# Kernel tuning notes

Measured on AMD Instinct MI355X. Metric: run time of the kernel, lower is better.

Reference implementation:

```python
import jax, jax.numpy as jnp
import numpy as np

EPS = 1e-5

def conv3x3(x, w, b):
    # x: [B,C,H,W], w: [O,I,3,3], padding=1 (SAME)
    y = jax.lax.conv_general_dilated(x, w, window_strides=(1, 1),
                                     padding=[(1, 1), (1, 1)],
                                     dimension_numbers=('NCHW', 'OIHW', 'NCHW'))
    return y + b[None, :, None, None]

def pool_block(x, k):
    # exact adaptive avg pool: 300 is divisible by the output size, block size k
    B, C, H, W = x.shape
    return x.reshape(B, C, H // k, k, W // k, k).mean(axis=(3, 5))

def upsample_nearest(x, k):
    # equivalent to the nested python-loop slice-assign in RIA
    return jnp.repeat(jnp.repeat(x, k, axis=2), k, axis=3)

def _conv_param(key, o, i):
    k1, k2 = jax.random.split(key)
    fan_in = i * 9
    w = jax.random.normal(k1, (o, i, 3, 3), jnp.float32) * np.sqrt(2.0 / fan_in)
    b = jax.random.normal(k2, (o,), jnp.float32) * 0.01
    return w, b

def setup_inputs() -> dict:
    key = jax.random.key(0)
    ks = jax.random.split(key, 16)
    inp = {}
    inp['im'] = jax.random.normal(ks[0], (32, 3, 300, 300), jnp.float32)
    inp['w1'], inp['b1'] = _conv_param(ks[1], 8, 3)
    inp['w2'], inp['b2'] = _conv_param(ks[2], 16, 8)
    inp['w3'], inp['b3'] = _conv_param(ks[3], 32, 16)
    inp['w4'], inp['b4'] = _conv_param(ks[4], 16, 32)
    inp['w5'], inp['b5'] = _conv_param(ks[5], 8, 16)
    inp['wc5'], inp['bc5'] = _conv_param(ks[6], 8, 16)
    inp['wc10'], inp['bc10'] = _conv_param(ks[7], 8, 16)
    inp['wc15'], inp['bc15'] = _conv_param(ks[8], 8, 16)
    inp['wg'], inp['bg'] = _conv_param(ks[9], 8, 24)
    inp['wm'], inp['bm'] = _conv_param(ks[10], 8, 24)
    inp['bn_w'] = jnp.ones((8,), jnp.float32)
    inp['bn_b'] = jnp.zeros((8,), jnp.float32)
    inp['w11'], inp['b11'] = _conv_param(ks[11], 1, 8)
    inp['gamma'] = jnp.full((1,), 0.3, jnp.float32)
    return inp

def reference(im, w1, b1, w2, b2, w3, b3, w4, b4, w5, b5,
              wc5, bc5, wc10, bc10, wc15, bc15,
              wg, bg, wm, bm, bn_w, bn_b, w11, b11, gamma):
    # attention conv chain 3->8->16->32->16->8
    x = conv3x3(im, w1, b1)
    x = conv3x3(x, w2, b2)
    x = conv3x3(x, w3, b3)
    x = conv3x3(x, w4, b4)
    x = conv3x3(x, w5, b5)  # [B,8,300,300]

    # RIA: triple-scale pooled context, nearest-upsampled and fused
    up5 = upsample_nearest(pool_block(x, 5), 5)
    up10 = upsample_nearest(pool_block(x, 10), 10)
    up15 = upsample_nearest(pool_block(x, 15), 15)
    c5 = conv3x3(jnp.concatenate([x, up5], axis=1), wc5, bc5)
    c10 = conv3x3(jnp.concatenate([x, up10], axis=1), wc10, bc10)
    c15 = conv3x3(jnp.concatenate([x, up15], axis=1), wc15, bc15)
    g_in = jnp.concatenate([c5, c10, c15], axis=1)  # [B,24,300,300]

    # gated conv (activation=None): conv(x) * sigmoid(mask_conv(x)), then BN (batch stats)
    gated = conv3x3(g_in, wg, bg) * jax.nn.sigmoid(conv3x3(g_in, wm, bm))
    mean = gated.mean(axis=(0, 2, 3), keepdims=True)
    var = gated.var(axis=(0, 2, 3), keepdims=True)
    gated = (gated - mean) * jax.lax.rsqrt(var + EPS)
    gated = gated * bn_w[None, :, None, None] + bn_b[None, :, None, None]

    # 8->1 conv, sigmoid attention map, residual gating with gamma
    att = jax.nn.sigmoid(conv3x3(gated, w11, b11))  # [B,1,300,300]
    out = gamma * (att * im) + (1.0 - gamma) * im
    return out
```

## Files before the change

kernel.cpp:

```cpp
#include <hip/hip_runtime.h>
#include <hip/hip_bf16.h>
#include <math.h>

typedef __hip_bfloat16 bf16;
typedef __attribute__((ext_vector_type(8))) __bf16 bf16x8;
typedef __attribute__((ext_vector_type(8))) unsigned short u16x8;
typedef __attribute__((ext_vector_type(4))) float f32x4;

#define H_ 300
#define W_ 300
#define HW_ 90000
#define NBATCH 32
#define NPART (NBATCH * 190)
#define NPB 95

__device__ __forceinline__ float b2f(unsigned short u) {
    return __uint_as_float((unsigned int)u << 16);
}
__device__ __forceinline__ unsigned short f2u(float v) {
    bf16 b = __float2bfloat16(v);
    return *reinterpret_cast<unsigned short*>(&b);
}
__device__ __forceinline__ float sigm(float x) { return 1.f / (1.f + __expf(-x)); }
__device__ __forceinline__ unsigned int packbf(float a, float b) {
    unsigned int r;
    asm("v_cvt_pk_bf16_f32 %0, %1, %2" : "=v"(r) : "v"(a), "v"(b));
    return r;
}

__global__ void pack_all_k(
    const float* __restrict__ w1, const float* __restrict__ w2,
    const float* __restrict__ w3, const float* __restrict__ w4,
    const float* __restrict__ w5, const float* __restrict__ wc5,
    const float* __restrict__ wc10, const float* __restrict__ wc15,
    const float* __restrict__ wg, const float* __restrict__ wm,
    unsigned short* __restrict__ WP)
{
    const float *a = nullptr, *bsec = nullptr;
    int cs = 999, CO = 0, CI = 0, CP = 8, NS = 3, NG = 1, off = 0, special = 0;
    switch (blockIdx.x) {
        case 0: a = w2;  CO = 16; CI = 8;  CP = 8;  NS = 3; off = 0;     break;
        case 1: a = w3;  CO = 32; CI = 16; CP = 16; NS = 5; NG = 2; off = 2048;  break;
        case 2: a = w4;  CO = 16; CI = 32; CP = 32; NS = 9; off = 8192;  break;
        case 3: a = w5;  CO = 8;  CI = 16; CP = 16; NS = 5; off = 13312; break;
        case 4: special = 1; CO = 32; CI = 32; CP = 32; NS = 9; NG = 2;
                off = 16384; break;
        case 5: a = wg; bsec = wm; cs = 8; CO = 16; CI = 24; CP = 32; NS = 9;
                off = 25600; break;
        case 6: a = w1;  CO = 8;  CI = 3;  CP = 8;  NS = 3; off = 30720; break;
    }
    unsigned short* outp = WP + off;
    int TPK = 32 / CP;
    int total = NS * NG * 512;
    for (int idx = threadIdx.x; idx < total; idx += 256) {
        int j = idx & 7;
        int lane = (idx >> 3) & 63;
        int g = (idx >> 9) % NG;
        int s = idx / (512 * NG);
        int col = lane & 15, kg = lane >> 4;
        int kk = kg * 8 + j;
        int tt = kk / CP, ci = kk % CP;
        int tap = s * TPK + tt;
        float v = 0.f;
        if (special) {
            int o = ci >> 3, c8 = ci & 7;
            int convid = (g == 0) ? (col < 8 ? 0 : 1) : (col < 8 ? 2 : -1);
            if (tap < 9 && convid >= 0) {
                const float* wc = (convid == 0) ? wc5 : (convid == 1) ? wc10 : wc15;
                int colc = col & 7;
                if (o == 0) v = wc[(colc * 16 + c8) * 9 + tap];
                else if (o == convid + 1) v = wc[(colc * 16 + 8 + c8) * 9 + tap];
            }
        } else {
            int co = g * 16 + col;
            if (tap < 9 && ci < CI && co < CO)
                v = (co >= cs) ? bsec[((co - cs) * CI + ci) * 9 + tap]
                               : a[(co * CI + ci) * 9 + tap];
        }
        outp[idx] = f2u(v);
    }
}

template <int CIN, int CINP, int COUT, int NGI, int MODE, int TH>
__global__ __launch_bounds__(256) void mfconv_k(
    const unsigned short* __restrict__ src,
    const unsigned short* __restrict__ wpack,
    const float* __restrict__ bias0, const float* __restrict__ bias1,
    unsigned short* __restrict__ out, int co_total, int co_off,
    float2* __restrict__ bnp, int img_base)
{
    constexpr int TPK = 32 / CINP;
    constexpr int NSTEP = (9 + TPK - 1) / TPK;
    constexpr int OCT = CINP / 8;
    constexpr int NPX = (TH + 2) * 34;

    __shared__ __align__(16) unsigned short s_in[OCT * NPX * 8];

    int b = blockIdx.z;
    int x0 = blockIdx.x * 32, y0 = blockIdx.y * TH;
    int tid = threadIdx.x;
    int lane = tid & 63, wv = tid >> 6;
    bool interior = (x0 >= 1) && (x0 + 32 < W_) && (y0 >= 1) && (y0 + TH < H_);

    if (MODE == 3) {
        const float* sf = reinterpret_cast<const float*>(src) + (size_t)b * 3 * HW_;
        if (interior) {
            const float* sf0 = sf + (size_t)(y0 - 1) * W_ + (x0 - 1);
            for (int e = tid; e < NPX; e += 256) {
                int y = e / 34;
                size_t o = (size_t)e + (size_t)y * 266;
                u16x8 v = {0, 0, 0, 0, 0, 0, 0, 0};
                v[0] = f2u(sf0[o]);
                v[1] = f2u(sf0[HW_ + o]);
                v[2] = f2u(sf0[2 * HW_ + o]);
                *(u16x8*)&s_in[e * 8] = v;
            }
        } else {
            for (int e = tid; e < NPX; e += 256) {
                int y = e / 34, x = e - y * 34;
                int gy = y0 + y - 1, gx = x0 + x - 1;
                u16x8 v = {0, 0, 0, 0, 0, 0, 0, 0};
                if (gy >= 0 && gy < H_ && gx >= 0 && gx < W_) {
                    size_t o = (size_t)gy * W_ + gx;
                    v[0] = f2u(sf[o]);
                    v[1] = f2u(sf[HW_ + o]);
                    v[2] = f2u(sf[2 * HW_ + o]);
                }
                *(u16x8*)&s_in[e * 8] = v;
            }
        }
    } else {
        const unsigned short* sb = src + (size_t)b * CIN * HW_;
        int oct = (OCT == 1) ? 0 : (wv % OCT);
        int phase = (OCT == 4) ? 0 : (wv / OCT);
        if (interior) {
            const unsigned short* sb0 =
                sb + ((size_t)(y0 - 1) * W_ + (x0 - 1)) * CIN + oct * 8;
            for (int px = lane + phase * 64; px < NPX; px += 256 / OCT) {
                int y = px / 34;
                u16x8 v;
                if (CIN == CINP || oct * 8 < CIN)
                    v = *(const u16x8*)&sb0[(size_t)(px + y * 266) * CIN];
                else
                    v = (u16x8){0, 0, 0, 0, 0, 0, 0, 0};
                *(u16x8*)&s_in[(oct * NPX + px) * 8] = v;
            }
        } else {
            for (int px = lane + phase * 64; px < NPX; px += 256 / OCT) {
                int y = px / 34, x = px - y * 34;
                int gy = y0 + y - 1, gx = x0 + x - 1;
                u16x8 v = {0, 0, 0, 0, 0, 0, 0, 0};
                if (gy >= 0 && gy < H_ && gx >= 0 && gx < W_ &&
                    (CIN == CINP || oct * 8 < CIN))
                    v = *(const u16x8*)&sb[((size_t)gy * W_ + gx) * CIN + oct * 8];
                *(u16x8*)&s_in[(oct * NPX + px) * 8] = v;
            }
        }
    }

    bf16x8 bw[NGI][NSTEP];
#pragma unroll
    for (int gi = 0; gi < NGI; ++gi)
#pragma unroll
        for (int s = 0; s < NSTEP; ++s)
            bw[gi][s] = *(const bf16x8*)&wpack[((s * NGI + gi) * 64 + lane) * 8];

    int col = lane & 15, kg = lane >> 4;

    float bias_r[NGI][4];
#pragma unroll
    for (int gi = 0; gi < NGI; ++gi)
#pragma unroll
        for (int r = 0; r < 4; ++r) {
            if (MODE == 2)
                bias_r[0][r] = (kg < 2) ? bias0[kg * 4 + r] : bias1[(kg - 2) * 4 + r];
            else {
                int co_l = gi * 16 + kg * 4 + r;
                bias_r[gi][r] = (co_l < COUT) ? bias0[co_l] : 0.f;
            }
        }

    float bs[4] = {0.f, 0.f, 0.f, 0.f}, bs2[4] = {0.f, 0.f, 0.f, 0.f};

    __syncthreads();

    if constexpr (OCT == 4) {
        int myb = wv * (TH / 4);
#pragma unroll
        for (int tx = 0; tx < 2; ++tx) {
            int pbase = kg * NPX + tx * 16 + col;
            bf16x8 fr[3][3];
#pragma unroll
            for (int r = 0; r < 2; ++r)
#pragma unroll
                for (int dx = 0; dx < 3; ++dx)
                    fr[r][dx] =
                        *(const bf16x8*)&s_in[(pbase + (myb + r) * 34 + dx) * 8];
#pragma unroll
            for (int ii = 0; ii < TH / 4; ++ii) {
#pragma unroll
                for (int dx = 0; dx < 3; ++dx)
                    fr[(ii + 2) % 3][dx] =
                        *(const bf16x8*)&s_in[(pbase + (myb + ii + 2) * 34 + dx) * 8];

                f32x4 acc[NGI];
#pragma unroll
                for (int gi = 0; gi < NGI; ++gi) acc[gi] = {0.f, 0.f, 0.f, 0.f};
#pragma unroll
                for (int dy = 0; dy < 3; ++dy)
#pragma unroll
                    for (int dx = 0; dx < 3; ++dx) {
                        bf16x8 a = fr[(ii + dy) % 3][dx];
#pragma unroll
                        for (int gi = 0; gi < NGI; ++gi)
                            acc[gi] = __builtin_amdgcn_mfma_f32_16x16x32_bf16(
                                bw[gi][dy * 3 + dx], a, acc[gi], 0, 0, 0);
                    }

                int gy = y0 + myb + ii;
                int gxx = x0 + tx * 16 + col;
                if (gy < H_) {
                    if (MODE == 2) {
                        float v0 = acc[0].x + bias_r[0][0];
                        float v1 = acc[0].y + bias_r[0][1];
                        float v2 = acc[0].z + bias_r[0][2];
                        float v3 = acc[0].w + bias_r[0][3];
                        float m0 = __shfl_xor(v0, 32), m1 = __shfl_xor(v1, 32);
                        float m2 = __shfl_xor(v2, 32), m3 = __shfl_xor(v3, 32);
                        if (kg < 2 && gxx < W_) {
                            float o0 = v0 * sigm(m0), o1 = v1 * sigm(m1);
                            float o2 = v2 * sigm(m2), o3 = v3 * sigm(m3);
                            uint2 st;
                            st.x = packbf(o0, o1);
                            st.y = packbf(o2, o3);
                            *(uint2*)&out[(((size_t)b * HW_ + (size_t)gy * W_ +
                                            gxx) * 8) + kg * 4] = st;
                            bs[0] += o0; bs2[0] += o0 * o0;
                            bs[1] += o1; bs2[1] += o1 * o1;
                            bs[2] += o2; bs2[2] += o2 * o2;
                            bs[3] += o3; bs2[3] += o3 * o3;
                        }
                    } else {
#pragma unroll
                        for (int gi = 0; gi < NGI; ++gi) {
                            int co_g = gi * 16 + kg * 4;
                            if (co_g < COUT && gxx < W_) {
                                uint2 st;
                                st.x = packbf(acc[gi].x + bias_r[gi][0],
                                              acc[gi].y + bias_r[gi][1]);
                                st.y = packbf(acc[gi].z + bias_r[gi][2],
                                              acc[gi].w + bias_r[gi][3]);
                                *(uint2*)&out[((size_t)b * HW_ +
                                               (size_t)gy * W_ + gxx) *
                                                  co_total + co_off + co_g] = st;
                            }
                        }
                    }
                }
            }
        }
    } else {
        int offs[NSTEP];
#pragma unroll
        for (int s = 0; s < NSTEP; ++s) {
            int t = s * TPK + kg / OCT;
            if (t > 8) t = 8;
            offs[s] = ((t / 3) * 34 + (t % 3)) * 8 + (kg % OCT) * (NPX * 8);
        }

#pragma unroll
        for (int i = 0; i < TH / 2; ++i) {
            int m = wv * (TH / 2) + i;
            int my = m >> 1, tx = m & 1;
            int gy = y0 + my;
            if (gy >= H_) continue;
            int base = (my * 34 + tx * 16 + col) * 8;

            f32x4 acc[NGI];
#pragma unroll
            for (int gi = 0; gi < NGI; ++gi) acc[gi] = {0.f, 0.f, 0.f, 0.f};
#pragma unroll
            for (int s = 0; s < NSTEP; ++s) {
                bf16x8 a = *(const bf16x8*)&s_in[base + offs[s]];
#pragma unroll
                for (int gi = 0; gi < NGI; ++gi)
                    acc[gi] = __builtin_amdgcn_mfma_f32_16x16x32_bf16(
                        bw[gi][s], a, acc[gi], 0, 0, 0);
            }

            int gxx = x0 + tx * 16 + col;
#pragma unroll
            for (int gi = 0; gi < NGI; ++gi) {
                int co_g = gi * 16 + kg * 4;
                if (co_g < COUT && gxx < W_) {
                    uint2 st;
                    st.x = packbf(acc[gi].x + bias_r[gi][0],
                                  acc[gi].y + bias_r[gi][1]);
                    st.y = packbf(acc[gi].z + bias_r[gi][2],
                                  acc[gi].w + bias_r[gi][3]);
                    *(uint2*)&out[((size_t)b * HW_ + (size_t)gy * W_ + gxx) *
                                      co_total + co_off + co_g] = st;
                }
            }
        }
    }

    if constexpr (MODE == 2) {
#pragma unroll
        for (int off = 1; off < 16; off <<= 1) {
#pragma unroll
            for (int r = 0; r < 4; ++r) {
                bs[r] += __shfl_xor(bs[r], off);
                bs2[r] += __shfl_xor(bs2[r], off);
            }
        }
        __shared__ float bsum[4][8], bsq[4][8];
        if (lane == 0) {
#pragma unroll
            for (int r = 0; r < 4; ++r) { bsum[wv][r] = bs[r]; bsq[wv][r] = bs2[r]; }
        }
        if (lane == 16) {
#pragma unroll
            for (int r = 0; r < 4; ++r) {
                bsum[wv][4 + r] = bs[r];
                bsq[wv][4 + r] = bs2[r];
            }
        }
        __syncthreads();
        if (tid < 8) {
            float s = 0.f, s2 = 0.f;
#pragma unroll
            for (int w = 0; w < 4; ++w) { s += bsum[w][tid]; s2 += bsq[w][tid]; }
            int bIdx = (img_base + b) * 190 + blockIdx.y * 10 + blockIdx.x;
            bnp[(size_t)bIdx * 8 + tid] = make_float2(s, s2);
        }
    }
}

__global__ __launch_bounds__(256) void convc3_k(
    const unsigned short* __restrict__ src,
    const unsigned short* __restrict__ p5, const unsigned short* __restrict__ p10,
    const unsigned short* __restrict__ p15,
    const unsigned short* __restrict__ wpack,
    const float* __restrict__ bc5, const float* __restrict__ bc10,
    const float* __restrict__ bc15, unsigned short* __restrict__ out)
{
    constexpr int TH = 16;
    constexpr int NPX = (TH + 2) * 34;
    __shared__ __align__(16) unsigned short s_in[4 * NPX * 8];

    int b = blockIdx.z;
    int x0 = blockIdx.x * 32, y0 = blockIdx.y * TH;
    int tid = threadIdx.x;
    int lane = tid & 63, wv = tid >> 6;
    bool interior = (x0 >= 1) && (x0 + 32 < W_) && (y0 >= 1) && (y0 + TH < H_);

    const unsigned short* sb = src + (size_t)b * 8 * HW_;
    const unsigned short* pb5 = p5 + (size_t)b * 8 * 3600;
    const unsigned short* pb10 = p10 + (size_t)b * 8 * 900;
    const unsigned short* pb15 = p15 + (size_t)b * 8 * 400;

    int oct = wv;
    if (interior) {
        const unsigned short* sb0 = sb + ((size_t)(y0 - 1) * W_ + (x0 - 1)) * 8;
        for (int px = lane; px < NPX; px += 64) {
            int y = px / 34;
            u16x8 v;
            if (oct == 0) {
                v = *(const u16x8*)&sb0[(size_t)(px + y * 266) * 8];
            } else {
                int x = px - y * 34;
                int gy = y0 - 1 + y, gx = x0 - 1 + x;
                const unsigned short* pp =
                    (oct == 1) ? &pb5[((size_t)(gy / 5) * 60 + gx / 5) * 8]
                    : (oct == 2) ? &pb10[((size_t)(gy / 10) * 30 + gx / 10) * 8]
                                 : &pb15[((size_t)(gy / 15) * 20 + gx / 15) * 8];
                v = *(const u16x8*)pp;
            }
            *(u16x8*)&s_in[(oct * NPX + px) * 8] = v;
        }
    } else {
        for (int px = lane; px < NPX; px += 64) {
            int y = px / 34, x = px - y * 34;
            int gy = y0 + y - 1, gx = x0 + x - 1;
            u16x8 v = {0, 0, 0, 0, 0, 0, 0, 0};
            if (gy >= 0 && gy < H_ && gx >= 0 && gx < W_) {
                if (oct == 0)
                    v = *(const u16x8*)&sb[((size_t)gy * W_ + gx) * 8];
                else if (oct == 1)
                    v = *(const u16x8*)&pb5[((size_t)(gy / 5) * 60 + gx / 5) * 8];
                else if (oct == 2)
                    v = *(const u16x8*)&pb10[((size_t)(gy / 10) * 30 + gx / 10) * 8];
                else
                    v = *(const u16x8*)&pb15[((size_t)(gy / 15) * 20 + gx / 15) * 8];
            }
            *(u16x8*)&s_in[(oct * NPX + px) * 8] = v;
        }
    }

    bf16x8 bw[2][9];
#pragma unroll
    for (int g = 0; g < 2; ++g)
#pragma unroll
        for (int s = 0; s < 9; ++s)
            bw[g][s] = *(const bf16x8*)&wpack[((s * 2 + g) * 64 + lane) * 8];

    int col = lane & 15, kg = lane >> 4;
    float bias_r[2][4];
#pragma unroll
    for (int r = 0; r < 4; ++r) {
        bias_r[0][r] = (kg < 2) ? bc5[kg * 4 + r] : bc10[(kg - 2) * 4 + r];
        bias_r[1][r] = (kg < 2) ? bc15[kg * 4 + r] : 0.f;
    }

    __syncthreads();

    int myb = wv * (TH / 4);
#pragma unroll
    for (int tx = 0; tx < 2; ++tx) {
        int pbase = kg * NPX + tx * 16 + col;
        bf16x8 fr[3][3];
#pragma unroll
        for (int r = 0; r < 2; ++r)
#pragma unroll
            for (int dx = 0; dx < 3; ++dx)
                fr[r][dx] = *(const bf16x8*)&s_in[(pbase + (myb + r) * 34 + dx) * 8];
#pragma unroll
        for (int ii = 0; ii < TH / 4; ++ii) {
#pragma unroll
            for (int dx = 0; dx < 3; ++dx)
                fr[(ii + 2) % 3][dx] =
                    *(const bf16x8*)&s_in[(pbase + (myb + ii + 2) * 34 + dx) * 8];

            f32x4 acc[2];
            acc[0] = {0.f, 0.f, 0.f, 0.f};
            acc[1] = {0.f, 0.f, 0.f, 0.f};
#pragma unroll
            for (int dy = 0; dy < 3; ++dy)
#pragma unroll
                for (int dx = 0; dx < 3; ++dx) {
                    bf16x8 a = fr[(ii + dy) % 3][dx];
                    acc[0] = __builtin_amdgcn_mfma_f32_16x16x32_bf16(
                        bw[0][dy * 3 + dx], a, acc[0], 0, 0, 0);
                    acc[1] = __builtin_amdgcn_mfma_f32_16x16x32_bf16(
                        bw[1][dy * 3 + dx], a, acc[1], 0, 0, 0);
                }

            int gy = y0 + myb + ii;
            int gxx = x0 + tx * 16 + col;
            if (gy < H_ && gxx < W_) {
                size_t pxo = ((size_t)b * HW_ + (size_t)gy * W_ + gxx) * 24;
                uint2 st0;
                st0.x = packbf(acc[0].x + bias_r[0][0], acc[0].y + bias_r[0][1]);
                st0.y = packbf(acc[0].z + bias_r[0][2], acc[0].w + bias_r[0][3]);
                *(uint2*)&out[pxo + kg * 4] = st0;
                if (kg < 2) {
                    uint2 st1;
                    st1.x = packbf(acc[1].x + bias_r[1][0], acc[1].y + bias_r[1][1]);
                    st1.y = packbf(acc[1].z + bias_r[1][2], acc[1].w + bias_r[1][3]);
                    *(uint2*)&out[pxo + 16 + kg * 4] = st1;
                }
            }
        }
    }
}

__global__ __launch_bounds__(256) void pool5_k(const unsigned short* __restrict__ x,
                                               unsigned short* __restrict__ p5,
                                               int n)
{
    int idx = blockIdx.x * 256 + threadIdx.x;
    if (idx >= n) return;
    int b = idx / 3600;
    int rem = idx - b * 3600;
    int i = rem / 60, j = rem - i * 60;
    const unsigned short* src =
        x + ((size_t)b * HW_ + (size_t)(i * 5) * W_ + j * 5) * 8;
    float ss[8] = {0, 0, 0, 0, 0, 0, 0, 0};
#pragma unroll
    for (int r = 0; r < 5; ++r)
#pragma unroll
        for (int c = 0; c < 5; ++c) {
            u16x8 v = *(const u16x8*)&src[((size_t)r * W_ + c) * 8];
#pragma unroll
            for (int k = 0; k < 8; ++k) ss[k] += b2f(v[k]);
        }
    uint4 st;
    st.x = packbf(ss[0] * 0.04f, ss[1] * 0.04f);
    st.y = packbf(ss[2] * 0.04f, ss[3] * 0.04f);
    st.z = packbf(ss[4] * 0.04f, ss[5] * 0.04f);
    st.w = packbf(ss[6] * 0.04f, ss[7] * 0.04f);
    *(uint4*)&p5[(size_t)idx * 8] = st;
}

template <int R, int OD>
__device__ __forceinline__ void poolr_body(const unsigned short* __restrict__ p5,
                                           unsigned short* __restrict__ po, int idx)
{
    int b = idx / (OD * OD);
    int rem = idx - b * OD * OD;
    int i = rem / OD, j = rem - i * OD;
    const unsigned short* src =
        p5 + ((size_t)b * 3600 + (size_t)(i * R) * 60 + j * R) * 8;
    float ss[8] = {0, 0, 0, 0, 0, 0, 0, 0};
    const float inv = 1.f / (R * R);
#pragma unroll
    for (int r = 0; r < R; ++r)
#pragma unroll
        for (int c = 0; c < R; ++c) {
            u16x8 v = *(const u16x8*)&src[((size_t)r * 60 + c) * 8];
#pragma unroll
            for (int k = 0; k < 8; ++k) ss[k] += b2f(v[k]);
        }
    uint4 st;
    st.x = packbf(ss[0] * inv, ss[1] * inv);
    st.y = packbf(ss[2] * inv, ss[3] * inv);
    st.z = packbf(ss[4] * inv, ss[5] * inv);
    st.w = packbf(ss[6] * inv, ss[7] * inv);
    *(uint4*)&po[(size_t)idx * 8] = st;
}

__global__ __launch_bounds__(256) void poolrs_k(const unsigned short* __restrict__ p5,
                                                unsigned short* __restrict__ p10,
                                                unsigned short* __restrict__ p15,
                                                int n10, int n15)
{
    int idx = blockIdx.x * 256 + threadIdx.x;
    if (idx < n10) {
        poolr_body<2, 30>(p5, p10, idx);
    } else {
        idx -= n10;
        if (idx < n15) poolr_body<3, 20>(p5, p15, idx);
    }
}

__global__ __launch_bounds__(256) void reduce_parts_k(
    const float2* __restrict__ parts, float2* __restrict__ parts2)
{
    int k = blockIdx.x;
    int tid = threadIdx.x;
    int c = tid & 7, j = tid >> 3;
    float s = 0.f, s2 = 0.f;
    for (int r = j; r < NPB; r += 32) {
        float2 p = parts[((size_t)k * NPB + r) * 8 + c];
        s += p.x;
// ... 121 lines not shown
                    float2 ov;
                    ov.x = iv.x * f[pr * 2 + 0];
                    ov.y = iv.y * f[pr * 2 + 1];
                    *(float2*)&ob[(size_t)(py + pr) * W_ + px] = ov;
                }
            }
        }
    }
}


extern "C" void kernel_launch(void* const* d_in, const int* in_sizes, int n_in,
                              void* d_out, int out_size, void* d_ws,
                              size_t ws_size, hipStream_t stream)
{
    (void)in_sizes; (void)n_in; (void)out_size;

    const float* im  = (const float*)d_in[0];
    const float* w1  = (const float*)d_in[1];
    const float* b1  = (const float*)d_in[2];
    const float* w2  = (const float*)d_in[3];
    const float* b2  = (const float*)d_in[4];
    const float* w3  = (const float*)d_in[5];
    const float* b3  = (const float*)d_in[6];
    const float* w4  = (const float*)d_in[7];
    const float* b4  = (const float*)d_in[8];
    const float* w5  = (const float*)d_in[9];
    const float* b5  = (const float*)d_in[10];
    const float* wc5 = (const float*)d_in[11];
    const float* bc5 = (const float*)d_in[12];
    const float* wc10= (const float*)d_in[13];
    const float* bc10= (const float*)d_in[14];
    const float* wc15= (const float*)d_in[15];
    const float* bc15= (const float*)d_in[16];
    const float* wg  = (const float*)d_in[17];
    const float* bg  = (const float*)d_in[18];
    const float* wm  = (const float*)d_in[19];
    const float* bm  = (const float*)d_in[20];
    const float* bnw = (const float*)d_in[21];
    const float* bnb = (const float*)d_in[22];
    const float* w11 = (const float*)d_in[23];
    const float* b11 = (const float*)d_in[24];
    const float* gam = (const float*)d_in[25];
    float* out = (float*)d_out;

    const size_t GATED_B = 46080000;
    const size_t PER_IMG = 1440000 + 2880000 + 5760000 + 57600 + 14400 + 6656;
    const size_t MISC    = 1048576;
    int c = 32;
    while (c > 1 && GATED_B + MISC + (size_t)c * PER_IMG + 2048 > ws_size)
        c >>= 1;

    char* p = (char*)d_ws;
    auto take = [&](size_t bytes) {
        char* r = p;
        p += (bytes + 255) & ~(size_t)255;
        return r;
    };
    unsigned short* GATED = (unsigned short*)take(GATED_B);
    unsigned short* A   = (unsigned short*)take((size_t)c * 1440000);
    unsigned short* Bb  = (unsigned short*)take((size_t)c * 2880000);
    unsigned short* C   = (unsigned short*)take((size_t)c * 5760000);
    unsigned short* P5  = (unsigned short*)take((size_t)c * 57600);
    unsigned short* P10 = (unsigned short*)take((size_t)c * 14400);
    unsigned short* P15 = (unsigned short*)take((size_t)c * 6656);
    float2* parts  = (float2*)take((size_t)NPART * 8 * sizeof(float2));
    float2* parts2 = (float2*)take(64 * 8 * sizeof(float2));
    float*  wfold  = (float*)take(512);
    unsigned short* WP = (unsigned short*)take(65536);

    unsigned short* PK2 = WP;
    unsigned short* PK3 = WP + 2048;
    unsigned short* PK4 = WP + 8192;
    unsigned short* PK5 = WP + 13312;
    unsigned short* PKc = WP + 16384;
    unsigned short* PKg = WP + 25600;
    unsigned short* PK1 = WP + 30720;

    dim3 blk(256);

    pack_all_k<<<dim3(7), blk, 0, stream>>>(w1, w2, w3, w4, w5, wc5, wc10, wc15,
                                            wg, wm, WP);

    for (int b0 = 0; b0 < NBATCH; b0 += c) {
        dim3 g32(10, 10, c);
        dim3 g16(10, 19, c);
        const float* imc = im + (size_t)b0 * 3 * HW_;

        mfconv_k<8, 8, 8, 1, 3, 32><<<g32, blk, 0, stream>>>(
            (const unsigned short*)imc, PK1, b1, nullptr, A, 8, 0, nullptr, 0);
        mfconv_k<8, 8, 16, 1, 0, 32><<<g32, blk, 0, stream>>>(
            A, PK2, b2, nullptr, Bb, 16, 0, nullptr, 0);
        mfconv_k<16, 16, 32, 2, 0, 32><<<g32, blk, 0, stream>>>(
            Bb, PK3, b3, nullptr, C, 32, 0, nullptr, 0);
        mfconv_k<32, 32, 16, 1, 0, 16><<<g16, blk, 0, stream>>>(
            C, PK4, b4, nullptr, Bb, 16, 0, nullptr, 0);
        mfconv_k<16, 16, 8, 1, 0, 32><<<g32, blk, 0, stream>>>(
            Bb, PK5, b5, nullptr, A, 8, 0, nullptr, 0);

        int n5 = c * 3600, n10 = c * 900, n15 = c * 400;
        pool5_k<<<dim3((n5 + 255) / 256), blk, 0, stream>>>(A, P5, n5);
        poolrs_k<<<dim3((n10 + n15 + 255) / 256), blk, 0, stream>>>(P5, P10, P15,
                                                                    n10, n15);

        convc3_k<<<g16, blk, 0, stream>>>(A, P5, P10, P15, PKc, bc5, bc10, bc15, C);

        mfconv_k<24, 32, 16, 1, 2, 16><<<g16, blk, 0, stream>>>(
            C, PKg, bg, bm, GATED + (size_t)b0 * HW_ * 8, 8, 0, parts, b0);
    }

    reduce_parts_k<<<dim3(64), blk, 0, stream>>>(parts, parts2);
    stats_fold_k<<<dim3(1), blk, 0, stream>>>(parts2, bnw, bnb, w11, b11, wfold);
    final_k<<<dim3(10, 10, NBATCH), blk, 0, stream>>>(GATED, wfold, im, gam,
                                                      out);
}
```

Before: 447.4 us.

## Double-buffer LDS tiles across two images in 32-channel conv kernels

The 32-input-channel conv kernels (conv4, the triple-context conv and the gated conv) now have each block process two images. The next image's halo tile is prefetched into registers while the current one is computed, then written to a second LDS buffer. The grid z dimension is halved, so global-load latency can overlap MFMA work. The cost is doubled shared memory and ten extra 16-byte registers per thread, which can lower occupancy, plus fewer blocks in flight.

Result: no change. 448.7 us (+0.3%).

```diff
diff --git a/kernel.cpp b/kernel.cpp
--- a/kernel.cpp
+++ b/kernel.cpp
@@ -81,82 +81,134 @@
     }
 }
 
-template <int CIN, int CINP, int COUT, int NGI, int MODE, int TH>
+template <int CIN, int CINP, int COUT, int NGI, int MODE, int TH, int PIPE>
 __global__ __launch_bounds__(256) void mfconv_k(
     const unsigned short* __restrict__ src,
     const unsigned short* __restrict__ wpack,
     const float* __restrict__ bias0, const float* __restrict__ bias1,
     unsigned short* __restrict__ out, int co_total, int co_off,
-    float2* __restrict__ bnp, int img_base)
+    float2* __restrict__ bnp, int img_base, int zimgs)
 {
     constexpr int TPK = 32 / CINP;
     constexpr int NSTEP = (9 + TPK - 1) / TPK;
     constexpr int OCT = CINP / 8;
     constexpr int NPX = (TH + 2) * 34;
-
-    __shared__ __align__(16) unsigned short s_in[OCT * NPX * 8];
-
-    int b = blockIdx.z;
+    constexpr int NIMG = PIPE ? 2 : 1;
+    static_assert(!PIPE || (OCT == 4 && TH == 16), "PIPE only for OCT4/TH16");
+
+    __shared__ __align__(16) unsigned short s_in[(PIPE ? 2 : 1) * OCT * NPX * 8];
+
+    int z = blockIdx.z;
     int x0 = blockIdx.x * 32, y0 = blockIdx.y * TH;
     int tid = threadIdx.x;
     int lane = tid & 63, wv = tid >> 6;
     bool interior = (x0 >= 1) && (x0 + 32 < W_) && (y0 >= 1) && (y0 + TH < H_);
 
-    if (MODE == 3) {
-        const float* sf = reinterpret_cast<const float*>(src) + (size_t)b * 3 * HW_;
-        if (interior) {
-            const float* sf0 = sf + (size_t)(y0 - 1) * W_ + (x0 - 1);
-            for (int e = tid; e < NPX; e += 256) {
-                int y = e / 34;
-                size_t o = (size_t)e + (size_t)y * 266;
-                u16x8 v = {0, 0, 0, 0, 0, 0, 0, 0};
-                v[0] = f2u(sf0[o]);
-                v[1] = f2u(sf0[HW_ + o]);
-                v[2] = f2u(sf0[2 * HW_ + o]);
-                *(u16x8*)&s_in[e * 8] = v;
+    int oct = (OCT == 1) ? 0 : (wv % OCT);
+    int phase = (OCT == 4) ? 0 : (wv / OCT);
+    bool voct = (CIN == CINP) || (oct * 8 < CIN);
+
+    auto stage_direct = [&](int b, unsigned short* sbuf) {
+        if (MODE == 3) {
+            const float* sf =
+                reinterpret_cast<const float*>(src) + (size_t)b * 3 * HW_;
+            if (interior) {
+                const float* sf0 = sf + (size_t)(y0 - 1) * W_ + (x0 - 1);
+                for (int e = tid; e < NPX; e += 256) {
+                    int y = e / 34;
+                    size_t o = (size_t)e + (size_t)y * 266;
+                    u16x8 v = {0, 0, 0, 0, 0, 0, 0, 0};
+                    v[0] = f2u(sf0[o]);
+                    v[1] = f2u(sf0[HW_ + o]);
+                    v[2] = f2u(sf0[2 * HW_ + o]);
+                    *(u16x8*)&sbuf[e * 8] = v;
+                }
+            } else {
+                for (int e = tid; e < NPX; e += 256) {
+                    int y = e / 34, x = e - y * 34;
+                    int gy = y0 + y - 1, gx = x0 + x - 1;
+                    u16x8 v = {0, 0, 0, 0, 0, 0, 0, 0};
+                    if (gy >= 0 && gy < H_ && gx >= 0 && gx < W_) {
+                        size_t o = (size_t)gy * W_ + gx;
+                        v[0] = f2u(sf[o]);
+                        v[1] = f2u(sf[HW_ + o]);
+                        v[2] = f2u(sf[2 * HW_ + o]);
+                    }
+                    *(u16x8*)&sbuf[e * 8] = v;
+                }
             }
         } else {
-            for (int e = tid; e < NPX; e += 256) {
-                int y = e / 34, x = e - y * 34;
-                int gy = y0 + y - 1, gx = x0 + x - 1;
-                u16x8 v = {0, 0, 0, 0, 0, 0, 0, 0};
-                if (gy >= 0 && gy < H_ && gx >= 0 && gx < W_) {
-                    size_t o = (size_t)gy * W_ + gx;
-                    v[0] = f2u(sf[o]);
-                    v[1] = f2u(sf[HW_ + o]);
-                    v[2] = f2u(sf[2 * HW_ + o]);
-                }
-                *(u16x8*)&s_in[e * 8] = v;
-            }
-        }
-    } else {
-        const unsigned short* sb = src + (size_t)b * CIN * HW_;
-        int oct = (OCT == 1) ? 0 : (wv % OCT);
-        int phase = (OCT == 4) ? 0 : (wv / OCT);
-        if (interior) {
-            const unsigned short* sb0 =
-                sb + ((size_t)(y0 - 1) * W_ + (x0 - 1)) * CIN + oct * 8;
-            for (int px = lane + phase * 64; px < NPX; px += 256 / OCT) {
-                int y = px / 34;
-                u16x8 v;
-                if (CIN == CINP || oct * 8 < CIN)
-                    v = *(const u16x8*)&sb0[(size_t)(px + y * 266) * CIN];
-                else
-                    v = (u16x8){0, 0, 0, 0, 0, 0, 0, 0};
-                *(u16x8*)&s_in[(oct * NPX + px) * 8] = v;
-            }
-        } else {
-            for (int px = lane + phase * 64; px < NPX; px += 256 / OCT) {
-                int y = px / 34, x = px - y * 34;
-                int gy = y0 + y - 1, gx = x0 + x - 1;
-                u16x8 v = {0, 0, 0, 0, 0, 0, 0, 0};
-                if (gy >= 0 && gy < H_ && gx >= 0 && gx < W_ &&
-                    (CIN == CINP || oct * 8 < CIN))
-                    v = *(const u16x8*)&sb[((size_t)gy * W_ + gx) * CIN + oct * 8];
-                *(u16x8*)&s_in[(oct * NPX + px) * 8] = v;
-            }
-        }
-    }
+            const unsigned short* sb = src + (size_t)b * CIN * HW_;
+            if (interior) {
+                const unsigned short* sb0 =
+                    sb + ((size_t)(y0 - 1) * W_ + (x0 - 1)) * CIN + oct * 8;
+                for (int px = lane + phase * 64; px < NPX; px += 256 / OCT) {
+                    int y = px / 34;
+                    u16x8 v;
+                    if (voct)
+                        v = *(const u16x8*)&sb0[(size_t)(px + y * 266) * CIN];
+                    else
+                        v = (u16x8){0, 0, 0, 0, 0, 0, 0, 0};
+                    *(u16x8*)&sbuf[(oct * NPX + px) * 8] = v;
+                }
+            } else {
+                for (int px = lane + phase * 64; px < NPX; px += 256 / OCT) {
+                    int y = px / 34, x = px - y * 34;
+                    int gy = y0 + y - 1, gx = x0 + x - 1;
+                    u16x8 v = {0, 0, 0, 0, 0, 0, 0, 0};
+                    if (gy >= 0 && gy < H_ && gx >= 0 && gx < W_ && voct)
+                        v = *(const u16x8*)&sb[((size_t)gy * W_ + gx) * CIN +
+                                               oct * 8];
+                    *(u16x8*)&sbuf[(oct * NPX + px) * 8] = v;
+                }
+            }
+        }
+    };
+
+    u16x8 pre[PIPE ? 10 : 1];
+    auto stage_load = [&](int b) {
+        if constexpr (PIPE) {
+            const unsigned short* sb = src + (size_t)b * CIN * HW_;
+            if (interior) {
+                const unsigned short* sb0 =
+                    sb + ((size_t)(y0 - 1) * W_ + (x0 - 1)) * CIN + oct * 8;
+#pragma unroll
+                for (int k = 0; k < 10; ++k) {
+                    int px = lane + k * 64;
+                    u16x8 v = {0, 0, 0, 0, 0, 0, 0, 0};
+                    if (px < NPX && voct) {
+                        int y = px / 34;
+                        v = *(const u16x8*)&sb0[(size_t)(px + y * 266) * CIN];
+                    }
+                    pre[k] = v;
+                }
+            } else {
+#pragma unroll
+                for (int k = 0; k < 10; ++k) {
+                    int px = lane + k * 64;
+                    u16x8 v = {0, 0, 0, 0, 0, 0, 0, 0};
+                    if (px < NPX) {
+                        int y = px / 34, x = px - y * 34;
+                        int gy = y0 + y - 1, gx = x0 + x - 1;
+                        if (gy >= 0 && gy < H_ && gx >= 0 && gx < W_ && voct)
+                            v = *(const u16x8*)&sb[((size_t)gy * W_ + gx) * CIN +
+                                                   oct * 8];
+                    }
+                    pre[k] = v;
+                }
+            }
+        }
+    };
+    auto stage_write = [&](int bsel) {
+        if constexpr (PIPE) {
+            unsigned short* sbuf = s_in + (size_t)bsel * (OCT * NPX * 8);
+#pragma unroll
+            for (int k = 0; k < 10; ++k) {
+                int px = lane + k * 64;
+                if (px < NPX) *(u16x8*)&sbuf[(oct * NPX + px) * 8] = pre[k];
+            }
+        }
+    };
 
     bf16x8 bw[NGI][NSTEP];
 #pragma unroll
@@ -180,223 +232,272 @@
             }
         }
 
-    float bs[4] = {0.f, 0.f, 0.f, 0.f}, bs2[4] = {0.f, 0.f, 0.f, 0.f};
-
+    if constexpr (PIPE) {
+        stage_load(z);
+        stage_write(0);
+    } else {
+        stage_direct(z, s_in);
+    }
     __syncthreads();
 
-    if constexpr (OCT == 4) {
-        int myb = wv * (TH / 4);
-#pragma unroll
-        for (int tx = 0; tx < 2; ++tx) {
-            int pbase = kg * NPX + tx * 16 + col;
-            bf16x8 fr[3][3];
-#pragma unroll
-            for (int r = 0; r < 2; ++r)
-#pragma unroll
-                for (int dx = 0; dx < 3; ++dx)
-                    fr[r][dx] =
-                        *(const bf16x8*)&s_in[(pbase + (myb + r) * 34 + dx) * 8];
-#pragma unroll
-            for (int ii = 0; ii < TH / 4; ++ii) {
-#pragma unroll
-                for (int dx = 0; dx < 3; ++dx)
-                    fr[(ii + 2) % 3][dx] =
-                        *(const bf16x8*)&s_in[(pbase + (myb + ii + 2) * 34 + dx) * 8];
-
-                f32x4 acc[NGI];
-#pragma unroll
-                for (int gi = 0; gi < NGI; ++gi) acc[gi] = {0.f, 0.f, 0.f, 0.f};
-#pragma unroll
-                for (int dy = 0; dy < 3; ++dy)
-#pragma unroll
-                    for (int dx = 0; dx < 3; ++dx) {
-                        bf16x8 a = fr[(ii + dy) % 3][dx];
-#pragma unroll
-                        for (int gi = 0; gi < NGI; ++gi)
-                            acc[gi] = __builtin_amdgcn_mfma_f32_16x16x32_bf16(
-                                bw[gi][dy * 3 + dx], a, acc[gi], 0, 0, 0);
-                    }
-
-                int gy = y0 + myb + ii;
-                int gxx = x0 + tx * 16 + col;
-                if (gy < H_) {
-                    if (MODE == 2) {
-                        float v0 = acc[0].x + bias_r[0][0];
-                        float v1 = acc[0].y + bias_r[0][1];
-                        float v2 = acc[0].z + bias_r[0][2];
-                        float v3 = acc[0].w + bias_r[0][3];
-                        float m0 = __shfl_xor(v0, 32), m1 = __shfl_xor(v1, 32);
-                        float m2 = __shfl_xor(v2, 32), m3 = __shfl_xor(v3, 32);
-                        if (kg < 2 && gxx < W_) {
-                            float o0 = v0 * sigm(m0), o1 = v1 * sigm(m1);
-                            float o2 = v2 * sigm(m2), o3 = v3 * sigm(m3);
-                            uint2 st;
-                            st.x = packbf(o0, o1);
-                            st.y = packbf(o2, o3);
-                            *(uint2*)&out[(((size_t)b * HW_ + (size_t)gy * W_ +
-                                            gxx) * 8) + kg * 4] = st;
-                            bs[0] += o0; bs2[0] += o0 * o0;
-                            bs[1] += o1; bs2[1] += o1 * o1;
-                            bs[2] += o2; bs2[2] += o2 * o2;
-                            bs[3] += o3; bs2[3] += o3 * o3;
+#pragma unroll
+    for (int i = 0; i < NIMG; ++i) {
+        int b = z + i * zimgs;
+        if (PIPE && i + 1 < NIMG) stage_load(z + (i + 1) * zimgs);
+        unsigned short* sbuf =
+            s_in + (PIPE ? (size_t)(i & 1) * (OCT * NPX * 8) : 0);
+
+        float bs[4] = {0.f, 0.f, 0.f, 0.f}, bs2[4] = {0.f, 0.f, 0.f, 0.f};
+
+        if constexpr (OCT == 4) {
+            int myb = wv * (TH / 4);
+#pragma unroll
+            for (int tx = 0; tx < 2; ++tx) {
+                int pbase = kg * NPX + tx * 16 + col;
+                bf16x8 fr[3][3];
+#pragma unroll
+                for (int r = 0; r < 2; ++r)
+#pragma unroll
+                    for (int dx = 0; dx < 3; ++dx)
+                        fr[r][dx] =
+                            *(const bf16x8*)&sbuf[(pbase + (myb + r) * 34 + dx) * 8];
+#pragma unroll
+                for (int ii = 0; ii < TH / 4; ++ii) {
+#pragma unroll
+                    for (int dx = 0; dx < 3; ++dx)
+                        fr[(ii + 2) % 3][dx] = *(const bf16x8*)&sbuf
+                            [(pbase + (myb + ii + 2) * 34 + dx) * 8];
+
+                    f32x4 acc[NGI];
+#pragma unroll
+                    for (int gi = 0; gi < NGI; ++gi) acc[gi] = {0.f, 0.f, 0.f, 0.f};
+#pragma unroll
+                    for (int dy = 0; dy < 3; ++dy)
+#pragma unroll
+                        for (int dx = 0; dx < 3; ++dx) {
+                            bf16x8 a = fr[(ii + dy) % 3][dx];
+#pragma unroll
+                            for (int gi = 0; gi < NGI; ++gi)
+                                acc[gi] = __builtin_amdgcn_mfma_f32_16x16x32_bf16(
+                                    bw[gi][dy * 3 + dx], a, acc[gi], 0, 0, 0);
                         }
-                    } else {
-#pragma unroll
-                        for (int gi = 0; gi < NGI; ++gi) {
-                            int co_g = gi * 16 + kg * 4;
-                            if (co_g < COUT && gxx < W_) {
+
+                    int gy = y0 + myb + ii;
+                    int gxx = x0 + tx * 16 + col;
+                    if (gy < H_) {
+                        if (MODE == 2) {
+                            float v0 = acc[0].x + bias_r[0][0];
+                            float v1 = acc[0].y + bias_r[0][1];
+                            float v2 = acc[0].z + bias_r[0][2];
+                            float v3 = acc[0].w + bias_r[0][3];
+                            float m0 = __shfl_xor(v0, 32), m1 = __shfl_xor(v1, 32);
+                            float m2 = __shfl_xor(v2, 32), m3 = __shfl_xor(v3, 32);
+                            if (kg < 2 && gxx < W_) {
+                                float o0 = v0 * sigm(m0), o1 = v1 * sigm(m1);
+                                float o2 = v2 * sigm(m2), o3 = v3 * sigm(m3);
                                 uint2 st;
-                                st.x = packbf(acc[gi].x + bias_r[gi][0],
-                                              acc[gi].y + bias_r[gi][1]);
-                                st.y = packbf(acc[gi].z + bias_r[gi][2],
-                                              acc[gi].w + bias_r[gi][3]);
-                                *(uint2*)&out[((size_t)b * HW_ +
-                                               (size_t)gy * W_ + gxx) *
-                                                  co_total + co_off + co_g] = st;
+                                st.x = packbf(o0, o1);
+                                st.y = packbf(o2, o3);
+                                *(uint2*)&out[(((size_t)b * HW_ +
+                                                (size_t)gy * W_ + gxx) * 8) +
+                                              kg * 4] = st;
+                                bs[0] += o0; bs2[0] += o0 * o0;
+                                bs[1] += o1; bs2[1] += o1 * o1;
+                                bs[2] += o2; bs2[2] += o2 * o2;
+                                bs[3] += o3; bs2[3] += o3 * o3;
+                            }
+                        } else {
+#pragma unroll
+                            for (int gi = 0; gi < NGI; ++gi) {
+                                int co_g = gi * 16 + kg * 4;
+                                if (co_g < COUT && gxx < W_) {
+                                    uint2 st;
+                                    st.x = packbf(acc[gi].x + bias_r[gi][0],
+                                                  acc[gi].y + bias_r[gi][1]);
+                                    st.y = packbf(acc[gi].z + bias_r[gi][2],
+                                                  acc[gi].w + bias_r[gi][3]);
+                                    *(uint2*)&out[((size_t)b * HW_ +
+                                                   (size_t)gy * W_ + gxx) *
+                                                      co_total + co_off + co_g] = st;
+                                }
                             }
                         }
                     }
                 }
             }
-        }
-    } else {
-        int offs[NSTEP];
-#pragma unroll
-        for (int s = 0; s < NSTEP; ++s) {
-            int t = s * TPK + kg / OCT;
-            if (t > 8) t = 8;
-            offs[s] = ((t / 3) * 34 + (t % 3)) * 8 + (kg % OCT) * (NPX * 8);
-        }
-
-#pragma unroll
-        for (int i = 0; i < TH / 2; ++i) {
-            int m = wv * (TH / 2) + i;
-            int my = m >> 1, tx = m & 1;
-            int gy = y0 + my;
-            if (gy >= H_) continue;
-            int base = (my * 34 + tx * 16 + col) * 8;
-
-            f32x4 acc[NGI];
-#pragma unroll
-            for (int gi = 0; gi < NGI; ++gi) acc[gi] = {0.f, 0.f, 0.f, 0.f};
+        } else {
+            int offs[NSTEP];
 #pragma unroll
             for (int s = 0; s < NSTEP; ++s) {
-                bf16x8 a = *(const bf16x8*)&s_in[base + offs[s]];
-#pragma unroll
-                for (int gi = 0; gi < NGI; ++gi)
-                    acc[gi] = __builtin_amdgcn_mfma_f32_16x16x32_bf16(
-                        bw[gi][s], a, acc[gi], 0, 0, 0);
-            }
-
-            int gxx = x0 + tx * 16 + col;
-#pragma unroll
-            for (int gi = 0; gi < NGI; ++gi) {
-                int co_g = gi * 16 + kg * 4;
-                if (co_g < COUT && gxx < W_) {
-                    uint2 st;
-                    st.x = packbf(acc[gi].x + bias_r[gi][0],
-                                  acc[gi].y + bias_r[gi][1]);
-                    st.y = packbf(acc[gi].z + bias_r[gi][2],
-                                  acc[gi].w + bias_r[gi][3]);
-                    *(uint2*)&out[((size_t)b * HW_ + (size_t)gy * W_ + gxx) *
-                                      co_total + co_off + co_g] = st;
-                }
-            }
-        }
-    }
-
-    if constexpr (MODE == 2) {
-#pragma unroll
-        for (int off = 1; off < 16; off <<= 1) {
-#pragma unroll
-            for (int r = 0; r < 4; ++r) {
-                bs[r] += __shfl_xor(bs[r], off);
-                bs2[r] += __shfl_xor(bs2[r], off);
-            }
-        }
-        __shared__ float bsum[4][8], bsq[4][8];
-        if (lane == 0) {
-#pragma unroll
-            for (int r = 0; r < 4; ++r) { bsum[wv][r] = bs[r]; bsq[wv][r] = bs2[r]; }
-        }
-        if (lane == 16) {
-#pragma unroll
-            for (int r = 0; r < 4; ++r) {
-                bsum[wv][4 + r] = bs[r];
-                bsq[wv][4 + r] = bs2[r];
-            }
-        }
-        __syncthreads();
-        if (tid < 8) {
-            float s = 0.f, s2 = 0.f;
-#pragma unroll
-            for (int w = 0; w < 4; ++w) { s += bsum[w][tid]; s2 += bsq[w][tid]; }
-            int bIdx = (img_base + b) * 190 + blockIdx.y * 10 + blockIdx.x;
-            bnp[(size_t)bIdx * 8 + tid] = make_float2(s, s2);
-        }
-    }
-}
-
+                int t = s * TPK + kg / OCT;
+                if (t > 8) t = 8;
+                offs[s] = ((t / 3) * 34 + (t % 3)) * 8 + (kg % OCT) * (NPX * 8);
+            }
+
+#pragma unroll
+            for (int i2 = 0; i2 < TH / 2; ++i2) {
+                int m = wv * (TH / 2) + i2;
+                int my = m >> 1, tx = m & 1;
+                int gy = y0 + my;
+                if (gy >= H_) continue;
+                int base = (my * 34 + tx * 16 + col) * 8;
+
+                f32x4 acc[NGI];
+#pragma unroll
+                for (int gi = 0; gi < NGI; ++gi) acc[gi] = {0.f, 0.f, 0.f, 0.f};
+#pragma unroll
+                for (int s = 0; s < NSTEP; ++s) {
+                    bf16x8 a = *(const bf16x8*)&sbuf[base + offs[s]];
+#pragma unroll
+                    for (int gi = 0; gi < NGI; ++gi)
+                        acc[gi] = __builtin_amdgcn_mfma_f32_16x16x32_bf16(
+                            bw[gi][s], a, acc[gi], 0, 0, 0);
+                }
+
+                int gxx = x0 + tx * 16 + col;
+#pragma unroll
+                for (int gi = 0; gi < NGI; ++gi) {
+                    int co_g = gi * 16 + kg * 4;
+                    if (co_g < COUT && gxx < W_) {
+                        uint2 st;
+                        st.x = packbf(acc[gi].x + bias_r[gi][0],
+                                      acc[gi].y + bias_r[gi][1]);
+                        st.y = packbf(acc[gi].z + bias_r[gi][2],
+                                      acc[gi].w + bias_r[gi][3]);
+                        *(uint2*)&out[((size_t)b * HW_ + (size_t)gy * W_ + gxx) *
+                                          co_total + co_off + co_g] = st;
+                    }
+                }
+            }
+        }
+
+        if constexpr (MODE == 2) {
+#pragma unroll
+            for (int off = 1; off < 16; off <<= 1) {
+#pragma unroll
+                for (int r = 0; r < 4; ++r) {
+                    bs[r] += __shfl_xor(bs[r], off);
+                    bs2[r] += __shfl_xor(bs2[r], off);
+                }
+            }
+            __shared__ float bsum[4][8], bsq[4][8];
+            if (lane == 0) {
+#pragma unroll
+                for (int r = 0; r < 4; ++r) {
+                    bsum[wv][r] = bs[r];
+                    bsq[wv][r] = bs2[r];
+                }
+            }
+            if (lane == 16) {
+#pragma unroll
+                for (int r = 0; r < 4; ++r) {
+                    bsum[wv][4 + r] = bs[r];
+                    bsq[wv][4 + r] = bs2[r];
+                }
+            }
+            __syncthreads();
+            if (tid < 8) {
+                float s = 0.f, s2 = 0.f;
+#pragma unroll
+                for (int w = 0; w < 4; ++w) { s += bsum[w][tid]; s2 += bsq[w][tid]; }
+                int bIdx = (img_base + b) * 190 + blockIdx.y * 10 + blockIdx.x;
+                bnp[(size_t)bIdx * 8 + tid] = make_float2(s, s2);
+            }
+        }
+
+        if (PIPE && i + 1 < NIMG) {
+            stage_write((i + 1) & 1);
+            __syncthreads();
+        }
+    }
+}
+
+template <int PIPE>
 __global__ __launch_bounds__(256) void convc3_k(
     const unsigned short* __restrict__ src,
     const unsigned short* __restrict__ p5, const unsigned short* __restrict__ p10,
     const unsigned short* __restrict__ p15,
     const unsigned short* __restrict__ wpack,
     const float* __restrict__ bc5, const float* __restrict__ bc10,
-    const float* __restrict__ bc15, unsigned short* __restrict__ out)
+    const float* __restrict__ bc15, unsigned short* __restrict__ out, int zimgs)
 {
     constexpr int TH = 16;
     constexpr int NPX = (TH + 2) * 34;
-    __shared__ __align__(16) unsigned short s_in[4 * NPX * 8];
-
-    int b = blockIdx.z;
+    constexpr int NIMG = PIPE ? 2 : 1;
+    __shared__ __align__(16) unsigned short s_in[(PIPE ? 2 : 1) * 4 * NPX * 8];
+
+    int z = blockIdx.z;
     int x0 = blockIdx.x * 32, y0 = blockIdx.y * TH;
     int tid = threadIdx.x;
     int lane = tid & 63, wv = tid >> 6;
     bool interior = (x0 >= 1) && (x0 + 32 < W_) && (y0 >= 1) && (y0 + TH < H_);
 
-    const unsigned short* sb = src + (size_t)b * 8 * HW_;
-    const unsigned short* pb5 = p5 + (size_t)b * 8 * 3600;
-    const unsigned short* pb10 = p10 + (size_t)b * 8 * 900;
-    const unsigned short* pb15 = p15 + (size_t)b * 8 * 400;
-
     int oct = wv;
-    if (interior) {
-        const unsigned short* sb0 = sb + ((size_t)(y0 - 1) * W_ + (x0 - 1)) * 8;
-        for (int px = lane; px < NPX; px += 64) {
-            int y = px / 34;
-            u16x8 v;
-            if (oct == 0) {
-                v = *(const u16x8*)&sb0[(size_t)(px + y * 266) * 8];
-            } else {
-                int x = px - y * 34;
-                int gy = y0 - 1 + y, gx = x0 - 1 + x;
-                const unsigned short* pp =
-                    (oct == 1) ? &pb5[((size_t)(gy / 5) * 60 + gx / 5) * 8]
-                    : (oct == 2) ? &pb10[((size_t)(gy / 10) * 30 + gx / 10) * 8]
-                                 : &pb15[((size_t)(gy / 15) * 20 + gx / 15) * 8];
-                v = *(const u16x8*)pp;
-            }
-            *(u16x8*)&s_in[(oct * NPX + px) * 8] = v;
-        }
-    } else {
-        for (int px = lane; px < NPX; px += 64) {
-            int y = px / 34, x = px - y * 34;
-            int gy = y0 + y - 1, gx = x0 + x - 1;
-            u16x8 v = {0, 0, 0, 0, 0, 0, 0, 0};
-            if (gy >= 0 && gy < H_ && gx >= 0 && gx < W_) {
-                if (oct == 0)
-                    v = *(const u16x8*)&sb[((size_t)gy * W_ + gx) * 8];
-                else if (oct == 1)
-                    v = *(const u16x8*)&pb5[((size_t)(gy / 5) * 60 + gx / 5) * 8];
-                else if (oct == 2)
-                    v = *(const u16x8*)&pb10[((size_t)(gy / 10) * 30 + gx / 10) * 8];
-                else
-                    v = *(const u16x8*)&pb15[((size_t)(gy / 15) * 20 + gx / 15) * 8];
-            }
-            *(u16x8*)&s_in[(oct * NPX + px) * 8] = v;
-        }
-    }
+
+    u16x8 pre[10];
+    auto stage_load = [&](int b) {
+        const unsigned short* sb = src + (size_t)b * 8 * HW_;
+        const unsigned short* pb5 = p5 + (size_t)b * 8 * 3600;
+        const unsigned short* pb10 = p10 + (size_t)b * 8 * 900;
+        const unsigned short* pb15 = p15 + (size_t)b * 8 * 400;
+        if (interior) {
+            const unsigned short* sb0 =
+                sb + ((size_t)(y0 - 1) * W_ + (x0 - 1)) * 8;
+#pragma unroll
+            for (int k = 0; k < 10; ++k) {
+                int px = lane + k * 64;
+                u16x8 v = {0, 0, 0, 0, 0, 0, 0, 0};
+                if (px < NPX) {
+                    int y = px / 34;
+                    if (oct == 0) {
+                        v = *(const u16x8*)&sb0[(size_t)(px + y * 266) * 8];
+                    } else {
+                        int x = px - y * 34;
+                        int gy = y0 - 1 + y, gx = x0 - 1 + x;
+                        const unsigned short* pp =
+                            (oct == 1) ? &pb5[((size_t)(gy / 5) * 60 + gx / 5) * 8]
+                            : (oct == 2)
+                                ? &pb10[((size_t)(gy / 10) * 30 + gx / 10) * 8]
+                                : &pb15[((size_t)(gy / 15) * 20 + gx / 15) * 8];
+                        v = *(const u16x8*)pp;
+                    }
+                }
+                pre[k] = v;
+            }
+        } else {
+#pragma unroll
+            for (int k = 0; k < 10; ++k) {
+                int px = lane + k * 64;
+                u16x8 v = {0, 0, 0, 0, 0, 0, 0, 0};
+                if (px < NPX) {
+                    int y = px / 34, x = px - y * 34;
+                    int gy = y0 + y - 1, gx = x0 + x - 1;
+                    if (gy >= 0 && gy < H_ && gx >= 0 && gx < W_) {
+                        if (oct == 0)
+                            v = *(const u16x8*)&sb[((size_t)gy * W_ + gx) * 8];
+                        else if (oct == 1)
+                            v = *(const u16x8*)&pb5[((size_t)(gy / 5) * 60 +
+                                                     gx / 5) * 8];
+                        else if (oct == 2)
+                            v = *(const u16x8*)&pb10[((size_t)(gy / 10) * 30 +
+                                                      gx / 10) * 8];
+                        else
+                            v = *(const u16x8*)&pb15[((size_t)(gy / 15) * 20 +
+                                                      gx / 15) * 8];
+                    }
+                }
+                pre[k] = v;
+            }
+        }
+    };
+    auto stage_write = [&](int bsel) {
+        unsigned short* sbuf = s_in + (size_t)bsel * (4 * NPX * 8);
+#pragma unroll
+        for (int k = 0; k < 10; ++k) {
+            int px = lane + k * 64;
+            if (px < NPX) *(u16x8*)&sbuf[(oct * NPX + px) * 8] = pre[k];
+        }
+    };
 
     bf16x8 bw[2][9];
 #pragma unroll
@@ -413,54 +514,71 @@
         bias_r[1][r] = (kg < 2) ? bc15[kg * 4 + r] : 0.f;
     }
 
+    stage_load(z);
+    stage_write(0);
     __syncthreads();
 
-    int myb = wv * (TH / 4);
-#pragma unroll
-    for (int tx = 0; tx < 2; ++tx) {
-        int pbase = kg * NPX + tx * 16 + col;
-        bf16x8 fr[3][3];
-#pragma unroll
-        for (int r = 0; r < 2; ++r)
-#pragma unroll
-            for (int dx = 0; dx < 3; ++dx)
-                fr[r][dx] = *(const bf16x8*)&s_in[(pbase + (myb + r) * 34 + dx) * 8];
-#pragma unroll
-        for (int ii = 0; ii < TH / 4; ++ii) {
-#pragma unroll
-            for (int dx = 0; dx < 3; ++dx)
-                fr[(ii + 2) % 3][dx] =
-                    *(const bf16x8*)&s_in[(pbase + (myb + ii + 2) * 34 + dx) * 8];
-
-            f32x4 acc[2];
-            acc[0] = {0.f, 0.f, 0.f, 0.f};
-            acc[1] = {0.f, 0.f, 0.f, 0.f};
-#pragma unroll
-            for (int dy = 0; dy < 3; ++dy)
-#pragma unroll
-                for (int dx = 0; dx < 3; ++dx) {
-                    bf16x8 a = fr[(ii + dy) % 3][dx];
-                    acc[0] = __builtin_amdgcn_mfma_f32_16x16x32_bf16(
-                        bw[0][dy * 3 + dx], a, acc[0], 0, 0, 0);
-                    acc[1] = __builtin_amdgcn_mfma_f32_16x16x32_bf16(
-                        bw[1][dy * 3 + dx], a, acc[1], 0, 0, 0);
-                }
-
-            int gy = y0 + myb + ii;
-            int gxx = x0 + tx * 16 + col;
-            if (gy < H_ && gxx < W_) {
-                size_t pxo = ((size_t)b * HW_ + (size_t)gy * W_ + gxx) * 24;
-                uint2 st0;
-                st0.x = packbf(acc[0].x + bias_r[0][0], acc[0].y + bias_r[0][1]);
-                st0.y = packbf(acc[0].z + bias_r[0][2], acc[0].w + bias_r[0][3]);
-                *(uint2*)&out[pxo + kg * 4] = st0;
-                if (kg < 2) {
-                    uint2 st1;
-                    st1.x = packbf(acc[1].x + bias_r[1][0], acc[1].y + bias_r[1][1]);
-                    st1.y = packbf(acc[1].z + bias_r[1][2], acc[1].w + bias_r[1][3]);
-                    *(uint2*)&out[pxo + 16 + kg * 4] = st1;
-                }
-            }
+#pragma unroll
+    for (int i = 0; i < NIMG; ++i) {
+        int b = z + i * zimgs;
+        if (PIPE && i + 1 < NIMG) stage_load(z + (i + 1) * zimgs);
+        unsigned short* sbuf = s_in + (size_t)(PIPE ? (i & 1) : 0) * (4 * NPX * 8);
+
+        int myb = wv * (TH / 4);
+#pragma unroll
+        for (int tx = 0; tx < 2; ++tx) {
+            int pbase = kg * NPX + tx * 16 + col;
+            bf16x8 fr[3][3];
+#pragma unroll
+            for (int r = 0; r < 2; ++r)
+#pragma unroll
+                for (int dx = 0; dx < 3; ++dx)
+                    fr[r][dx] =
+                        *(const bf16x8*)&sbuf[(pbase + (myb + r) * 34 + dx) * 8];
+#pragma unroll
+            for (int ii = 0; ii < TH / 4; ++ii) {
+#pragma unroll
+                for (int dx = 0; dx < 3; ++dx)
+                    fr[(ii + 2) % 3][dx] =
+                        *(const bf16x8*)&sbuf[(pbase + (myb + ii + 2) * 34 + dx) * 8];
+
+                f32x4 acc[2];
+                acc[0] = {0.f, 0.f, 0.f, 0.f};
+                acc[1] = {0.f, 0.f, 0.f, 0.f};
+#pragma unroll
+                for (int dy = 0; dy < 3; ++dy)
+#pragma unroll
+                    for (int dx = 0; dx < 3; ++dx) {
+                        bf16x8 a = fr[(ii + dy) % 3][dx];
+                        acc[0] = __builtin_amdgcn_mfma_f32_16x16x32_bf16(
+                            bw[0][dy * 3 + dx], a, acc[0], 0, 0, 0);
+                        acc[1] = __builtin_amdgcn_mfma_f32_16x16x32_bf16(
+                            bw[1][dy * 3 + dx], a, acc[1], 0, 0, 0);
+                    }
+
+                int gy = y0 + myb + ii;
+                int gxx = x0 + tx * 16 + col;
+                if (gy < H_ && gxx < W_) {
+                    size_t pxo = ((size_t)b * HW_ + (size_t)gy * W_ + gxx) * 24;
+                    uint2 st0;
+                    st0.x = packbf(acc[0].x + bias_r[0][0], acc[0].y + bias_r[0][1]);
+                    st0.y = packbf(acc[0].z + bias_r[0][2], acc[0].w + bias_r[0][3]);
+                    *(uint2*)&out[pxo + kg * 4] = st0;
+                    if (kg < 2) {
+                        uint2 st1;
+                        st1.x = packbf(acc[1].x + bias_r[1][0],
+                                       acc[1].y + bias_r[1][1]);
+                        st1.y = packbf(acc[1].z + bias_r[1][2],
+                                       acc[1].w + bias_r[1][3]);
+                        *(uint2*)&out[pxo + 16 + kg * 4] = st1;
+                    }
+                }
+            }
+        }
+
+        if (PIPE && i + 1 < NIMG) {
+            stage_write((i + 1) & 1);
+            __syncthreads();
         }
     }
 }
@@ -748,31 +866,50 @@
     pack_all_k<<<dim3(7), blk, 0, stream>>>(w1, w2, w3, w4, w5, wc5, wc10, wc15,
                                             wg, wm, WP);
 
+    int zi = (c >= 2) ? (c / 2) : 1;
+    bool pipe = (c >= 2);
+
     for (int b0 = 0; b0 < NBATCH; b0 += c) {
         dim3 g32(10, 10, c);
         dim3 g16(10, 19, c);
+        dim3 g16p(10, 19, zi);
         const float* imc = im + (size_t)b0 * 3 * HW_;
 
-        mfconv_k<8, 8, 8, 1, 3, 32><<<g32, blk, 0, stream>>>(
-            (const unsigned short*)imc, PK1, b1, nullptr, A, 8, 0, nullptr, 0);
-        mfconv_k<8, 8, 16, 1, 0, 32><<<g32, blk, 0, stream>>>(
-            A, PK2, b2, nullptr, Bb, 16, 0, nullptr, 0);
-        mfconv_k<16, 16, 32, 2, 0, 32><<<g32, blk, 0, stream>>>(
-            Bb, PK3, b3, nullptr, C, 32, 0, nullptr, 0);
-        mfconv_k<32, 32, 16, 1, 0, 16><<<g16, blk, 0, stream>>>(
-            C, PK4, b4, nullptr, Bb, 16, 0, nullptr, 0);
-        mfconv_k<16, 16, 8, 1, 0, 32><<<g32, blk, 0, stream>>>(
-            Bb, PK5, b5, nullptr, A, 8, 0, nullptr, 0);
+        mfconv_k<8, 8, 8, 1, 3, 32, 0><<<g32, blk, 0, stream>>>(
+            (const unsigned short*)imc, PK1, b1, nullptr, A, 8, 0, nullptr, 0, c);
+        mfconv_k<8, 8, 16, 1, 0, 32, 0><<<g32, blk, 0, stream>>>(
+            A, PK2, b2, nullptr, Bb, 16, 0, nullptr, 0, c);
+        mfconv_k<16, 16, 32, 2, 0, 32, 0><<<g32, blk, 0, stream>>>(
+            Bb, PK3, b3, nullptr, C, 32, 0, nullptr, 0, c);
+
+        if (pipe)
+            mfconv_k<32, 32, 16, 1, 0, 16, 1><<<g16p, blk, 0, stream>>>(
+                C, PK4, b4, nullptr, Bb, 16, 0, nullptr, 0, zi);
+        else
+            mfconv_k<32, 32, 16, 1, 0, 16, 0><<<g16, blk, 0, stream>>>(
+                C, PK4, b4, nullptr, Bb, 16, 0, nullptr, 0, c);
+
+        mfconv_k<16, 16, 8, 1, 0, 32, 0><<<g32, blk, 0, stream>>>(
+            Bb, PK5, b5, nullptr, A, 8, 0, nullptr, 0, c);
 
         int n5 = c * 3600, n10 = c * 900, n15 = c * 400;
         pool5_k<<<dim3((n5 + 255) / 256), blk, 0, stream>>>(A, P5, n5);
         poolrs_k<<<dim3((n10 + n15 + 255) / 256), blk, 0, stream>>>(P5, P10, P15,
                                                                     n10, n15);
 
-        convc3_k<<<g16, blk, 0, stream>>>(A, P5, P10, P15, PKc, bc5, bc10, bc15, C);
-
-        mfconv_k<24, 32, 16, 1, 2, 16><<<g16, blk, 0, stream>>>(
-            C, PKg, bg, bm, GATED + (size_t)b0 * HW_ * 8, 8, 0, parts, b0);
+        if (pipe)
+            convc3_k<1><<<g16p, blk, 0, stream>>>(A, P5, P10, P15, PKc, bc5,
+                                                  bc10, bc15, C, zi);
+        else
+            convc3_k<0><<<g16, blk, 0, stream>>>(A, P5, P10, P15, PKc, bc5,
+                                                 bc10, bc15, C, c);
+
+        if (pipe)
+            mfconv_k<24, 32, 16, 1, 2, 16, 1><<<g16p, blk, 0, stream>>>(
+                C, PKg, bg, bm, GATED + (size_t)b0 * HW_ * 8, 8, 0, parts, b0, zi);
+        else
+            mfconv_k<24, 32, 16, 1, 2, 16, 0><<<g16, blk, 0, stream>>>(
+                C, PKg, bg, bm, GATED + (size_t)b0 * HW_ * 8, 8, 0, parts, b0, c);
     }
 
     reduce_parts_k<<<dim3(64), blk, 0, stream>>>(parts, parts2);
```
